# Kernel tuning notes

Hardware: AMD Instinct MI355X
Metric: run time of the kernel (lower is better)

The kernel has to match this reference:

```python
import jax, jax.numpy as jnp
import numpy as np

E = 512
H = 8
D = E // H  # head_dim = 64
SCALE = D ** -0.5
NEG_INF = float('-inf')


def layer_norm(x, g, b, eps=1e-5):
    mu = jnp.mean(x, axis=-1, keepdims=True)
    var = jnp.var(x, axis=-1, keepdims=True)
    return (x - mu) * jax.lax.rsqrt(var + eps) * g + b


def setup_inputs() -> dict:
    key = jax.random.key(0)
    ks = jax.random.split(key, 16)
    B, Q, K = 4, 2048, 2048
    inp = {
        'query': jax.random.normal(ks[0], (B, Q, E), jnp.float32),
        'key_value': jax.random.normal(ks[1], (B, K, E), jnp.float32),
        'kv_mask': jax.random.randint(ks[2], (B, K), 0, 2) > 0,
        'sparse_mask': jax.random.randint(ks[3], (B, Q, K), 0, 2) > 0,
        'ln_q_g': jnp.ones((E,), jnp.float32),
        'ln_q_b': jnp.zeros((E,), jnp.float32),
        'ln_kv_g': jnp.ones((E,), jnp.float32),
        'ln_kv_b': jnp.zeros((E,), jnp.float32),
        # Linear weights stored as (in, out): y = x @ W + b
        'Wq': jax.random.normal(ks[4], (E, E), jnp.float32) * (E ** -0.5),
        'bq': jnp.zeros((E,), jnp.float32),
        'Wk': jax.random.normal(ks[5], (E, E), jnp.float32) * (E ** -0.5),
        'bk': jnp.zeros((E,), jnp.float32),
        'Wv': jax.random.normal(ks[6], (E, E), jnp.float32) * (E ** -0.5),
        'bv': jnp.zeros((E,), jnp.float32),
        'Wo': jax.random.normal(ks[7], (E, E), jnp.float32) * (E ** -0.5),
        'bo': jnp.zeros((E,), jnp.float32),
    }
    return inp


def reference(query, key_value, kv_mask, sparse_mask,
              ln_q_g, ln_q_b, ln_kv_g, ln_kv_b,
              Wq, bq, Wk, bk, Wv, bv, Wo, bo):
    B, Qn, _ = query.shape
    Kn = key_value.shape[1]
    qn = layer_norm(query, ln_q_g, ln_q_b)
    kvn = layer_norm(key_value, ln_kv_g, ln_kv_b)
    q = (qn @ Wq + bq).reshape(B, Qn, H, D)
    k = (kvn @ Wk + bk).reshape(B, Kn, H, D)
    v = (kvn @ Wv + bv).reshape(B, Kn, H, D)
    # scores: [B, H, Q, K]
    scores = jnp.einsum('bqhd,bkhd->bhqk', q, k) * SCALE
    mask = kv_mask[:, None, None, :] & sparse_mask[:, None, :, :]
    scores = jnp.where(mask, scores, NEG_INF)
    attn = jax.nn.softmax(scores, axis=-1)
    # nan_to_num(0): rows with no valid key -> all-zero weights
    valid_row = jnp.any(mask, axis=-1, keepdims=True)
    attn = jnp.where(valid_row, attn, 0.0)
    out = jnp.einsum('bhqk,bkhd->bqhd', attn, v).reshape(B, Qn, E)
    return out @ Wo + bo
```

## Files before the change

kernel.cpp:

```cpp
#include <hip/hip_runtime.h>
#include <hip/hip_bf16.h>
#include <math.h>

typedef unsigned short ushort_t;
typedef __attribute__((ext_vector_type(8))) __bf16 bf16x8;
typedef __attribute__((ext_vector_type(4))) float f32x4;
typedef __attribute__((ext_vector_type(16))) float f32x16;
typedef __attribute__((ext_vector_type(4))) unsigned int u32x4;

#define E_DIM 512
#define HEADS 8
#define HD 64
#define SEQ 2048
#define NROWS 8192
#define NEGF (-1e30f)
#define QSCALE 0.18033688011112042f

static __device__ __forceinline__ unsigned short f2b(float f) {
  unsigned int x;
  __builtin_memcpy(&x, &f, 4);
  x += 0x7fffu + ((x >> 16) & 1u);
  return (unsigned short)(x >> 16);
}

static __device__ __forceinline__ int swz(int row, int col) {
  return row * 64 + ((((col >> 3) ^ (row & 7)) & 7) << 3) + (col & 7);
}

static __device__ __forceinline__ void gl2lds16(const ushort_t* g, ushort_t* s) {
#if __has_builtin(__builtin_amdgcn_global_load_lds)
  __builtin_amdgcn_global_load_lds(
      (const __attribute__((address_space(1))) unsigned int*)(uintptr_t)g,
      (__attribute__((address_space(3))) unsigned int*)(uintptr_t)s,
      16, 0, 0);
#else
  int l = threadIdx.x & 63;
  *(u32x4*)(s + l * 8) = *(const u32x4*)g;
#endif
}

__launch_bounds__(256)
__global__ void prep_kernel(const float* __restrict__ Wq, const float* __restrict__ Wk,
                            const float* __restrict__ Wv, const float* __restrict__ Wo,
                            ushort_t* __restrict__ WT,
                            const int* __restrict__ kvm, const int* __restrict__ sp,
                            unsigned long long* __restrict__ bits,
                            const float* __restrict__ xq, const float* __restrict__ xkv,
                            const float* __restrict__ gq, const float* __restrict__ bq,
                            const float* __restrict__ gkv, const float* __restrict__ bkv,
                            ushort_t* __restrict__ yq, ushort_t* __restrict__ ykv) {
  int blk = blockIdx.x;
  int t = threadIdx.x;
  if (blk < 1024) {
    int z = blk >> 8, rem = blk & 255;
    const float* in = (z == 0) ? Wq : (z == 1) ? Wk : (z == 2) ? Wv : Wo;
    ushort_t* o = WT + (size_t)z * E_DIM * E_DIM;
    __shared__ float tile[32 * 33];
    int tx = t & 31, ty = t >> 5;
    int n0 = (rem & 15) * 32, k0 = (rem >> 4) * 32;
#pragma unroll
    for (int i = 0; i < 4; ++i) {
      int k = ty + i * 8;
      tile[k * 33 + tx] = in[(k0 + k) * E_DIM + n0 + tx];
    }
    __syncthreads();
#pragma unroll
    for (int i = 0; i < 4; ++i) {
      int n = ty + i * 8;
      o[(n0 + n) * E_DIM + k0 + tx] = f2b(tile[tx * 33 + n]);
    }
  } else if (blk < 3072) {
    int w = t >> 6, l = t & 63;
    int row = (blk - 1024) * 4 + w;
    int b = row >> 11;
    const int* sprow = sp + ((size_t)row << 11);
    const int* kvrow = kvm + (b << 11);
    unsigned long long* out = bits + ((size_t)row << 5);
#pragma unroll 4
    for (int it = 0; it < 32; ++it) {
      int k = it * 64 + l;
      unsigned long long m = __ballot(sprow[k] != 0 && kvrow[k] != 0);
      if (l == 0) out[it] = m;
    }
  } else {
    int idx = blk - 3072;
    int which = idx >> 11;
    const float* x = which ? xkv : xq;
    const float* g = which ? gkv : gq;
    const float* bb = which ? bkv : bq;
    ushort_t* y = which ? ykv : yq;
    int w = t >> 6, l = t & 63;
    int row = (idx & 2047) * 4 + w;
    f32x4 x0 = *(const f32x4*)&x[row * E_DIM + l * 8];
    f32x4 x1 = *(const f32x4*)&x[row * E_DIM + l * 8 + 4];
    float xf[8], s = 0.f, ss = 0.f;
#pragma unroll
    for (int j = 0; j < 8; ++j) {
      xf[j] = (j < 4) ? x0[j] : x1[j - 4];
      s += xf[j];
      ss += xf[j] * xf[j];
    }
#pragma unroll
    for (int off = 32; off > 0; off >>= 1) {
      s += __shfl_xor(s, off);
      ss += __shfl_xor(ss, off);
    }
    float mu = s * (1.f / 512.f);
    float var = fmaxf(ss * (1.f / 512.f) - mu * mu, 0.f);
    float rs = rsqrtf(var + 1e-5f);
    f32x4 g0 = *(const f32x4*)&g[l * 8];
    f32x4 g1 = *(const f32x4*)&g[l * 8 + 4];
    f32x4 b0 = *(const f32x4*)&bb[l * 8];
    f32x4 b1 = *(const f32x4*)&bb[l * 8 + 4];
#pragma unroll
    for (int j = 0; j < 8; ++j) {
      float gv = (j < 4) ? g0[j] : g1[j - 4];
      float bv = (j < 4) ? b0[j] : b1[j - 4];
      y[row * E_DIM + l * 8 + j] = f2b((xf[j] - mu) * rs * gv + bv);
    }
  }
}

template <int MODE>
static __device__ __forceinline__ void gemm_core128(ushort_t* lA, ushort_t* lB,
                                                    const ushort_t* __restrict__ A,
                                                    const ushort_t* __restrict__ WT,
                                                    const float* __restrict__ bias,
                                                    void* Cv, float scale, int m0, int n0) {
  int t = threadIdx.x, w = t >> 6, l = t & 63;
  int quad = l >> 4, l15 = l & 15;
  int wm_ = w >> 1, wn_ = w & 1;
  int csrc = ((l & 7) ^ (l >> 3)) * 8;
  int rln = l >> 3;

  f32x4 acc[4][4] = {};
  for (int kk = 0; kk < E_DIM; kk += 64) {
    __syncthreads();
#pragma unroll
    for (int i = 0; i < 4; ++i) {
      int r0 = i * 32 + w * 8;
      gl2lds16(&A[(size_t)(m0 + r0 + rln) * E_DIM + kk + csrc], &lA[r0 * 64]);
      gl2lds16(&WT[(size_t)(n0 + r0 + rln) * E_DIM + kk + csrc], &lB[r0 * 64]);
    }
    __syncthreads();
#pragma unroll
    for (int ks = 0; ks < 2; ++ks) {
      bf16x8 af[4], bf[4];
#pragma unroll
      for (int mt = 0; mt < 4; ++mt)
        af[mt] = *(const bf16x8*)&lA[swz(wm_ * 64 + mt * 16 + l15, ks * 32 + quad * 8)];
#pragma unroll
      for (int nt = 0; nt < 4; ++nt)
        bf[nt] = *(const bf16x8*)&lB[swz(wn_ * 64 + nt * 16 + l15, ks * 32 + quad * 8)];
#pragma unroll
      for (int mt = 0; mt < 4; ++mt)
#pragma unroll
        for (int nt = 0; nt < 4; ++nt)
          acc[mt][nt] = __builtin_amdgcn_mfma_f32_16x16x32_bf16(af[mt], bf[nt], acc[mt][nt], 0, 0, 0);
    }
  }

#pragma unroll
  for (int nt = 0; nt < 4; ++nt) {
    int col = n0 + wn_ * 64 + nt * 16 + l15;
    float bv = bias[col];
    if constexpr (MODE == 2) {
      int h = col >> 6, d = col & 63;
#pragma unroll
      for (int mt = 0; mt < 4; ++mt) {
        int row = m0 + wm_ * 64 + mt * 16 + quad * 4;
        int b = row >> 11, k = row & 2047;
        union { ushort_t u[4]; uint2 v; } pk;
#pragma unroll
        for (int r = 0; r < 4; ++r) pk.u[r] = f2b(acc[mt][nt][r] + bv);
        *(uint2*)&((ushort_t*)Cv)[((((size_t)(b * HEADS + h)) * HD + d) << 11) + k] = pk.v;
      }
    } else {
#pragma unroll
      for (int mt = 0; mt < 4; ++mt) {
#pragma unroll
        for (int r = 0; r < 4; ++r) {
          int rowm = m0 + wm_ * 64 + mt * 16 + quad * 4 + r;
          float val = (acc[mt][nt][r] + bv) * scale;
          if constexpr (MODE == 0)
            ((ushort_t*)Cv)[rowm * E_DIM + col] = f2b(val);
          else
            ((float*)Cv)[rowm * E_DIM + col] = val;
        }
      }
    }
  }
}

__launch_bounds__(256)
__global__ void gemm128_bf16(const ushort_t* __restrict__ A, const ushort_t* __restrict__ WT,
                             const float* __restrict__ bias, ushort_t* __restrict__ C, float scale) {
  __shared__ ushort_t lA[128 * 64];
  __shared__ ushort_t lB[128 * 64];
  gemm_core128<0>(lA, lB, A, WT, bias, C, scale, blockIdx.x * 128, blockIdx.y * 128);
}

__launch_bounds__(256)
__global__ void gemm128_f32(const ushort_t* __restrict__ A, const ushort_t* __restrict__ WT,
                            const float* __restrict__ bias, float* __restrict__ C) {
  __shared__ ushort_t lA[128 * 64];
  __shared__ ushort_t lB[128 * 64];
  gemm_core128<1>(lA, lB, A, WT, bias, C, 1.f, blockIdx.x * 128, blockIdx.y * 128);
}

__launch_bounds__(256)
__global__ void proj2_kernel(const ushort_t* __restrict__ qn, const ushort_t* __restrict__ WTq,
                             const float* __restrict__ bq, ushort_t* __restrict__ qp,
                             const ushort_t* __restrict__ kvn, const ushort_t* __restrict__ WTv,
                             const float* __restrict__ bv, ushort_t* __restrict__ Vt) {
  __shared__ ushort_t lA[128 * 64];
  __shared__ ushort_t lB[128 * 64];
  int m0 = blockIdx.x * 128, n0 = blockIdx.y * 128;
  if (blockIdx.z == 0) gemm_core128<0>(lA, lB, qn, WTq, bq, qp, QSCALE, m0, n0);
  else                 gemm_core128<2>(lA, lB, kvn, WTv, bv, Vt, 1.f, m0, n0);
}

__launch_bounds__(256)
__global__ void attn_kernel(const ushort_t* __restrict__ Qp, const ushort_t* __restrict__ Kp,
                            const ushort_t* __restrict__ Vt,
                            const unsigned long long* __restrict__ bits,
                            ushort_t* __restrict__ ctx) {
  __shared__ ushort_t sQ[128 * 64];
  __shared__ ushort_t sK[64 * 64];
  __shared__ ushort_t sVt[64 * 64];
  __shared__ ushort_t sP[128 * 64];
  int t = threadIdx.x, w = t >> 6, l = t & 63;
  int l31 = l & 31, half = l >> 5;
  int q0 = blockIdx.x * 128;
  int h = blockIdx.y;
  int b = blockIdx.z;
  int bh = b * HEADS + h;
  int myq = w * 32 + l31;
  int csrc = ((l & 7) ^ (l >> 3)) * 8;
  int rln = l >> 3;

#pragma unroll
  for (int it = 0; it < 4; ++it) {
    int r0 = it * 32 + w * 8;
    gl2lds16(&Qp[(size_t)(b * SEQ + q0 + r0 + rln) * E_DIM + h * HD + csrc], &sQ[r0 * 64]);
  }

  const unsigned long long* mrow = bits + ((size_t)(b * SEQ + q0 + myq) << 5);
  float lsum = 0.f;
  f32x16 o0 = {}, o1 = {};
  bf16x8 qf[4];

  for (int kt = 0; kt < 32; ++kt) {
    int k0 = kt * 64;
    __syncthreads();
#pragma unroll
    for (int it = 0; it < 2; ++it) {
      int r0 = it * 32 + w * 8;
      gl2lds16(&Kp[(size_t)(b * SEQ + k0 + r0 + rln) * E_DIM + h * HD + csrc], &sK[r0 * 64]);
      gl2lds16(&Vt[((size_t)bh * HD + r0 + rln) * SEQ + k0 + csrc], &sVt[r0 * 64]);
    }
    __syncthreads();
    if (kt == 0) {
#pragma unroll
      for (int ds = 0; ds < 4; ++ds)
        qf[ds] = *(const bf16x8*)&sQ[swz(myq, ds * 16 + 8 * half)];
    }

    f32x16 s0 = {}, s1 = {};
#pragma unroll
    for (int ds = 0; ds < 4; ++ds) {
      bf16x8 kf0 = *(const bf16x8*)&sK[swz(l31, ds * 16 + 8 * half)];
      bf16x8 kf1 = *(const bf16x8*)&sK[swz(32 + l31, ds * 16 + 8 * half)];
      s0 = __builtin_amdgcn_mfma_f32_32x32x16_bf16(kf0, qf[ds], s0, 0, 0, 0);
      s1 = __builtin_amdgcn_mfma_f32_32x32x16_bf16(kf1, qf[ds], s1, 0, 0, 0);
    }

    unsigned long long wmask = mrow[kt];
#pragma unroll
    for (int kt2 = 0; kt2 < 2; ++kt2) {
      const f32x16& sv = kt2 ? s1 : s0;
      unsigned h32 = ((unsigned)(wmask >> (32 * kt2))) >> (4 * half);
#pragma unroll
      for (int g = 0; g < 4; ++g) {
        unsigned gb = h32 >> (8 * g);
        union { ushort_t u[4]; uint2 v; } pk;
#pragma unroll
        for (int r = 0; r < 4; ++r) {
          float smv = ((gb >> r) & 1u) ? sv[g * 4 + r] : NEGF;
          float pv = exp2f(smv);
          pk.u[r] = (unsigned short)(__float_as_uint(pv) >> 16);
          lsum += pv;
        }
        *(uint2*)&sP[swz(myq, kt2 * 32 + g * 8 + 4 * half)] = pk.v;
      }
    }

#pragma unroll
    for (int ksp = 0; ksp < 4; ++ksp) {
      bf16x8 pf = *(const bf16x8*)&sP[swz(myq, ksp * 16 + 8 * half)];
      bf16x8 vf0 = *(const bf16x8*)&sVt[swz(l31, ksp * 16 + 8 * half)];
      bf16x8 vf1 = *(const bf16x8*)&sVt[swz(32 + l31, ksp * 16 + 8 * half)];
      o0 = __builtin_amdgcn_mfma_f32_32x32x16_bf16(vf0, pf, o0, 0, 0, 0);
      o1 = __builtin_amdgcn_mfma_f32_32x32x16_bf16(vf1, pf, o1, 0, 0, 0);
    }
  }

  lsum += __shfl_xor(lsum, 32);
  float inv = (lsum > 0.f) ? 1.f / lsum : 0.f;
  size_t base = (size_t)(b * SEQ + q0 + myq) * E_DIM + h * HD;
#pragma unroll
  for (int dt = 0; dt < 2; ++dt) {
    const f32x16& oo = dt ? o1 : o0;
#pragma unroll
    for (int g = 0; g < 4; ++g) {
      union { ushort_t u[4]; uint2 v; } ov;
#pragma unroll
      for (int r = 0; r < 4; ++r) ov.u[r] = f2b(oo[g * 4 + r] * inv);
      *(uint2*)&ctx[base + dt * 32 + g * 8 + 4 * half] = ov.v;
    }
  }
}

extern "C" void kernel_launch(void* const* d_in, const int* in_sizes, int n_in,
                              void* d_out, int out_size, void* d_ws, size_t ws_size,
                              hipStream_t stream) {
  const float* query     = (const float*)d_in[0];
  const float* key_value = (const float*)d_in[1];
  const int*   kv_mask   = (const int*)d_in[2];
  const int*   sp_mask   = (const int*)d_in[3];
  const float* ln_q_g  = (const float*)d_in[4];
  const float* ln_q_b  = (const float*)d_in[5];
  const float* ln_kv_g = (const float*)d_in[6];
  const float* ln_kv_b = (const float*)d_in[7];
  const float* Wq = (const float*)d_in[8];
  const float* bq = (const float*)d_in[9];
  const float* Wk = (const float*)d_in[10];
  const float* bk = (const float*)d_in[11];
  const float* Wv = (const float*)d_in[12];
  const float* bv = (const float*)d_in[13];
  const float* Wo = (const float*)d_in[14];
  const float* bo = (const float*)d_in[15];

  const size_t NB = (size_t)NROWS * E_DIM;
  char* ws = (char*)d_ws;
  ushort_t* bufA = (ushort_t*)ws;
  ushort_t* bufB = bufA + NB;
  ushort_t* WT   = bufB + NB;
  ushort_t* WTq = WT;
  ushort_t* WTk = WTq + E_DIM * E_DIM;
  ushort_t* WTv = WTk + E_DIM * E_DIM;
  ushort_t* WTo = WTv + E_DIM * E_DIM;
  unsigned long long* bits = (unsigned long long*)(WTo + E_DIM * E_DIM);

  ushort_t* dlo = (ushort_t*)d_out;
  ushort_t* dhi = dlo + NB;

  prep_kernel<<<7168, 256, 0, stream>>>(Wq, Wk, Wv, Wo, WT, kv_mask, sp_mask, bits,
                                        query, key_value, ln_q_g, ln_q_b, ln_kv_g, ln_kv_b,
                                        dlo, bufA);

  proj2_kernel<<<dim3(64, 4, 2), 256, 0, stream>>>(dlo, WTq, bq, dhi,
                                                   bufA, WTv, bv, bufB);

  gemm128_bf16<<<dim3(64, 4), 256, 0, stream>>>(bufA, WTk, bk, dlo, 1.f);

  attn_kernel<<<dim3(16, HEADS, 4), 256, 0, stream>>>(dhi, dlo, bufB, bits, bufA);

  gemm128_f32<<<dim3(64, 4), 256, 0, stream>>>(bufA, WTo, bo, (float*)d_out);
}
```

Before: 285.3 us.

## Double-buffer K/V tiles and keep P in registers via permlane swaps

Double-buffers the K and V LDS tiles so the next tile's global-to-LDS load is issued before the current tile is computed, leaving one barrier per iteration instead of two. It also drops the shared-memory round trip for the probability tile P: values are packed with v_cvt_pk_bf16_f32 and rearranged across lane halves with v_permlane32_swap into MFMA operand layout. It also splits the row-sum into four accumulators and raises wave priority around the MFMA blocks. The cost is more register pressure, reliance on inline asm specific to gfx950, and bf16 rounding of P that now rounds to nearest instead of truncating.

New measurement: 287.4 us. About the same (+0.7%).

```diff
diff --git a/kernel.cpp b/kernel.cpp
--- a/kernel.cpp
+++ b/kernel.cpp
@@ -21,6 +21,12 @@
   __builtin_memcpy(&x, &f, 4);
   x += 0x7fffu + ((x >> 16) & 1u);
   return (unsigned short)(x >> 16);
+}
+
+static __device__ __forceinline__ unsigned cvt_pk_bf16(float lo, float hi) {
+  unsigned r;
+  asm("v_cvt_pk_bf16_f32 %0, %1, %2" : "=v"(r) : "v"(lo), "v"(hi));
+  return r;
 }
 
 static __device__ __forceinline__ int swz(int row, int col) {
@@ -226,9 +232,8 @@
                             const unsigned long long* __restrict__ bits,
                             ushort_t* __restrict__ ctx) {
   __shared__ ushort_t sQ[128 * 64];
-  __shared__ ushort_t sK[64 * 64];
-  __shared__ ushort_t sVt[64 * 64];
-  __shared__ ushort_t sP[128 * 64];
+  __shared__ ushort_t sK[2][64 * 64];
+  __shared__ ushort_t sV[2][64 * 64];
   int t = threadIdx.x, w = t >> 6, l = t & 63;
   int l31 = l & 31, half = l >> 5;
   int q0 = blockIdx.x * 128;
@@ -244,67 +249,92 @@
     int r0 = it * 32 + w * 8;
     gl2lds16(&Qp[(size_t)(b * SEQ + q0 + r0 + rln) * E_DIM + h * HD + csrc], &sQ[r0 * 64]);
   }
+#pragma unroll
+  for (int it = 0; it < 2; ++it) {
+    int r0 = it * 32 + w * 8;
+    gl2lds16(&Kp[(size_t)(b * SEQ + r0 + rln) * E_DIM + h * HD + csrc], &sK[0][r0 * 64]);
+    gl2lds16(&Vt[((size_t)bh * HD + r0 + rln) * SEQ + csrc], &sV[0][r0 * 64]);
+  }
+  __syncthreads();
+
+  bf16x8 qf[4];
+#pragma unroll
+  for (int ds = 0; ds < 4; ++ds)
+    qf[ds] = *(const bf16x8*)&sQ[swz(myq, ds * 16 + 8 * half)];
 
   const unsigned long long* mrow = bits + ((size_t)(b * SEQ + q0 + myq) << 5);
-  float lsum = 0.f;
+  float ls0 = 0.f, ls1 = 0.f, ls2 = 0.f, ls3 = 0.f;
   f32x16 o0 = {}, o1 = {};
-  bf16x8 qf[4];
+  int cur = 0;
 
   for (int kt = 0; kt < 32; ++kt) {
-    int k0 = kt * 64;
-    __syncthreads();
-#pragma unroll
-    for (int it = 0; it < 2; ++it) {
-      int r0 = it * 32 + w * 8;
-      gl2lds16(&Kp[(size_t)(b * SEQ + k0 + r0 + rln) * E_DIM + h * HD + csrc], &sK[r0 * 64]);
-      gl2lds16(&Vt[((size_t)bh * HD + r0 + rln) * SEQ + k0 + csrc], &sVt[r0 * 64]);
-    }
-    __syncthreads();
-    if (kt == 0) {
-#pragma unroll
-      for (int ds = 0; ds < 4; ++ds)
-        qf[ds] = *(const bf16x8*)&sQ[swz(myq, ds * 16 + 8 * half)];
+    unsigned long long wmask = mrow[kt];
+
+    if (kt < 31) {
+      int k0 = (kt + 1) * 64;
+      int nxt = cur ^ 1;
+#pragma unroll
+      for (int it = 0; it < 2; ++it) {
+        int r0 = it * 32 + w * 8;
+        gl2lds16(&Kp[(size_t)(b * SEQ + k0 + r0 + rln) * E_DIM + h * HD + csrc], &sK[nxt][r0 * 64]);
+        gl2lds16(&Vt[((size_t)bh * HD + r0 + rln) * SEQ + k0 + csrc], &sV[nxt][r0 * 64]);
+      }
     }
 
     f32x16 s0 = {}, s1 = {};
+    __builtin_amdgcn_s_setprio(1);
 #pragma unroll
     for (int ds = 0; ds < 4; ++ds) {
-      bf16x8 kf0 = *(const bf16x8*)&sK[swz(l31, ds * 16 + 8 * half)];
-      bf16x8 kf1 = *(const bf16x8*)&sK[swz(32 + l31, ds * 16 + 8 * half)];
+      bf16x8 kf0 = *(const bf16x8*)&sK[cur][swz(l31, ds * 16 + 8 * half)];
+      bf16x8 kf1 = *(const bf16x8*)&sK[cur][swz(32 + l31, ds * 16 + 8 * half)];
       s0 = __builtin_amdgcn_mfma_f32_32x32x16_bf16(kf0, qf[ds], s0, 0, 0, 0);
       s1 = __builtin_amdgcn_mfma_f32_32x32x16_bf16(kf1, qf[ds], s1, 0, 0, 0);
     }
-
-    unsigned long long wmask = mrow[kt];
+    __builtin_amdgcn_s_setprio(0);
+
+    bf16x8 pf[4];
 #pragma unroll
     for (int kt2 = 0; kt2 < 2; ++kt2) {
       const f32x16& sv = kt2 ? s1 : s0;
       unsigned h32 = ((unsigned)(wmask >> (32 * kt2))) >> (4 * half);
+      unsigned wa[4], wb[4];
 #pragma unroll
       for (int g = 0; g < 4; ++g) {
         unsigned gb = h32 >> (8 * g);
-        union { ushort_t u[4]; uint2 v; } pk;
-#pragma unroll
-        for (int r = 0; r < 4; ++r) {
-          float smv = ((gb >> r) & 1u) ? sv[g * 4 + r] : NEGF;
-          float pv = exp2f(smv);
-          pk.u[r] = (unsigned short)(__float_as_uint(pv) >> 16);
-          lsum += pv;
-        }
-        *(uint2*)&sP[swz(myq, kt2 * 32 + g * 8 + 4 * half)] = pk.v;
+        float p0 = exp2f((gb & 1u)        ? sv[g * 4 + 0] : NEGF);
+        float p1 = exp2f(((gb >> 1) & 1u) ? sv[g * 4 + 1] : NEGF);
+        float p2 = exp2f(((gb >> 2) & 1u) ? sv[g * 4 + 2] : NEGF);
+        float p3 = exp2f(((gb >> 3) & 1u) ? sv[g * 4 + 3] : NEGF);
+        ls0 += p0; ls1 += p1; ls2 += p2; ls3 += p3;
+        wa[g] = cvt_pk_bf16(p0, p1);
+        wb[g] = cvt_pk_bf16(p2, p3);
       }
-    }
-
+      asm("v_permlane32_swap_b32 %0, %1" : "+v"(wa[0]), "+v"(wa[1]));
+      asm("v_permlane32_swap_b32 %0, %1" : "+v"(wb[0]), "+v"(wb[1]));
+      asm("v_permlane32_swap_b32 %0, %1" : "+v"(wa[2]), "+v"(wa[3]));
+      asm("v_permlane32_swap_b32 %0, %1" : "+v"(wb[2]), "+v"(wb[3]));
+      union { unsigned u[4]; bf16x8 v; } f0, f1;
+      f0.u[0] = wa[0]; f0.u[1] = wb[0]; f0.u[2] = wa[1]; f0.u[3] = wb[1];
+      f1.u[0] = wa[2]; f1.u[1] = wb[2]; f1.u[2] = wa[3]; f1.u[3] = wb[3];
+      pf[kt2 * 2 + 0] = f0.v;
+      pf[kt2 * 2 + 1] = f1.v;
+    }
+
+    __builtin_amdgcn_s_setprio(1);
 #pragma unroll
     for (int ksp = 0; ksp < 4; ++ksp) {
-      bf16x8 pf = *(const bf16x8*)&sP[swz(myq, ksp * 16 + 8 * half)];
-      bf16x8 vf0 = *(const bf16x8*)&sVt[swz(l31, ksp * 16 + 8 * half)];
-      bf16x8 vf1 = *(const bf16x8*)&sVt[swz(32 + l31, ksp * 16 + 8 * half)];
-      o0 = __builtin_amdgcn_mfma_f32_32x32x16_bf16(vf0, pf, o0, 0, 0, 0);
-      o1 = __builtin_amdgcn_mfma_f32_32x32x16_bf16(vf1, pf, o1, 0, 0, 0);
-    }
-  }
-
+      bf16x8 vf0 = *(const bf16x8*)&sV[cur][swz(l31, ksp * 16 + 8 * half)];
+      bf16x8 vf1 = *(const bf16x8*)&sV[cur][swz(32 + l31, ksp * 16 + 8 * half)];
+      o0 = __builtin_amdgcn_mfma_f32_32x32x16_bf16(vf0, pf[ksp], o0, 0, 0, 0);
+      o1 = __builtin_amdgcn_mfma_f32_32x32x16_bf16(vf1, pf[ksp], o1, 0, 0, 0);
+    }
+    __builtin_amdgcn_s_setprio(0);
+
+    __syncthreads();
+    cur ^= 1;
+  }
+
+  float lsum = (ls0 + ls1) + (ls2 + ls3);
   lsum += __shfl_xor(lsum, 32);
   float inv = (lsum > 0.f) ? 1.f / lsum : 0.f;
   size_t base = (size_t)(b * SEQ + q0 + myq) * E_DIM + h * HD;
```
